# Kernel tuning notes

Hardware: AMD Instinct MI355X
Metric: run time of the kernel (lower is better)

Reference implementation:

```python
import jax, jax.numpy as jnp
import numpy as np

_EPS = 1e-7  # clamp for BCE numerical validity (torch BCE asserts input in [0,1])


def _erode6(m):
    """Binary erosion with 3D 6-connectivity (scipy generate_binary_structure(3,1)),
    border_value=0. m: [B, C, D, H, W] float in {0,1}. Erosion of a binary mask with
    a cross structuring element == min over the voxel and its 6 face neighbors."""
    p = jnp.pad(m, ((0, 0), (0, 0), (1, 1), (1, 1), (1, 1)))  # zero pad == border_value 0
    e = p[:, :, 1:-1, 1:-1, 1:-1]
    e = jnp.minimum(e, p[:, :, :-2, 1:-1, 1:-1])
    e = jnp.minimum(e, p[:, :, 2:, 1:-1, 1:-1])
    e = jnp.minimum(e, p[:, :, 1:-1, :-2, 1:-1])
    e = jnp.minimum(e, p[:, :, 1:-1, 2:, 1:-1])
    e = jnp.minimum(e, p[:, :, 1:-1, 1:-1, :-2])
    e = jnp.minimum(e, p[:, :, 1:-1, 1:-1, 2:])
    return e


def _boundary_map(mask):
    """Faithful to _get_boundary_map: binarize (astype(bool) == nonzero), erode each
    channel, boundary = float_mask - eroded, sum over channels. Returns [B, D, H, W]."""
    mask = mask.astype(jnp.float32)
    mb = (mask != 0).astype(jnp.float32)
    eroded = _erode6(mb)
    return jnp.sum(mask - eroded, axis=1)


def setup_inputs() -> dict:
    key = jax.random.key(0)
    k1, k2 = jax.random.split(key)
    B, C, D, H, W = 4, 2, 128, 192, 192
    inputs = jax.random.normal(k1, (B, C, D, H, W), dtype=jnp.float32)
    targets = jax.random.randint(k2, (B, C, D, H, W), 0, 2, dtype=jnp.int32)
    return {"inputs": inputs, "targets": targets}


def reference(inputs, targets):
    p = jax.nn.sigmoid(inputs)
    boundary_targets = _boundary_map(targets)
    boundary_inputs = _boundary_map(p)
    # binary_cross_entropy(boundary_inputs, boundary_targets, reduction='none')
    bi = jnp.clip(boundary_inputs, _EPS, 1.0 - _EPS)
    loss = -(boundary_targets * jnp.log(bi) + (1.0 - boundary_targets) * jnp.log1p(-bi))
    return jnp.mean(loss)  # reduction='mean'
```

## Files before the change

### kernel.cpp

```cpp
#include <hip/hip_runtime.h>
#include <math.h>

#define Bq 4
#define Dd 128
#define Hh 192
#define Ww 192

typedef unsigned long long ull;

constexpr int HW    = Hh * Ww;
constexpr int DHW   = Dd * HW;
constexpr int CDHW  = 2 * DHW;
constexpr int WPP   = HW / 64;
constexpr int WPC   = Dd * WPP;
constexpr int TOTW  = Bq * 2 * WPC;
constexpr int TOTV  = TOTW * 64;
constexpr float INV_N = 1.0f / 18874368.0f;

#define C0f 1.00000005e-07f
#define C1f 16.1180955f

__device__ __forceinline__ float edge_loss(float x0, float x1, float bt) {
    float p0 = 1.f / (1.f + expf(-x0));
    float p1 = 1.f / (1.f + expf(-x1));
    float bi = fminf(fmaxf(p0 + p1, 1e-7f), 1.f - 1e-7f);
    return -(bt * logf(bi) + (1.f - bt) * log1pf(-bi));
}

__device__ __forceinline__ void block_reduce_atomic(float loss, float* out) {
    #pragma unroll
    for (int off = 32; off > 0; off >>= 1)
        loss += __shfl_down(loss, off, 64);
    __shared__ float s[4];
    int lane = threadIdx.x & 63;
    int wid  = threadIdx.x >> 6;
    if (lane == 0) s[wid] = loss;
    __syncthreads();
    if (threadIdx.x == 0)
        atomicAdd(out, (s[0] + s[1] + s[2] + s[3]) * INV_N);
}

__global__ __launch_bounds__(256) void pack_kernel(
    const int* __restrict__ t, ull* __restrict__ packed)
{
    const int lane  = threadIdx.x & 63;
    const int gwave = (blockIdx.x * 256 + threadIdx.x) >> 6;
    const int base  = gwave * 4096;
    const int* p = t + base + lane;
    ull word = 0;
    #pragma unroll
    for (int k = 0; k < 64; ++k) {
        ull bal = __ballot(p[k * 64] != 0);
        if (lane == k) word = bal;
    }
    packed[gwave * 64 + lane] = word;
}

constexpr int NROWSI = Bq * 126 * 190;

__global__ __launch_bounds__(256) void interior_kernel(
    const float* __restrict__ x, const ull* __restrict__ pk,
    float* __restrict__ out)
{
    int rid = blockIdx.x * 256 + threadIdx.x;
    float loss = 0.f;
    if (rid < NROWSI) {
        int h = 1 + rid % 190;
        int d = 1 + (rid / 190) % 126;
        int b = rid / (190 * 126);

        const ull* q0 = pk + (b * 2) * WPC + d * WPP + h * 3;
        const ull* q1 = q0 + WPC;

        ull c00 = q0[0],   c01 = q0[1],      c02 = q0[2];
        ull n00 = q0[-3],  n01 = q0[-2],     n02 = q0[-1];
        ull s00 = q0[3],   s01 = q0[4],      s02 = q0[5];
        ull f00 = q0[-WPP],f01 = q0[-WPP+1], f02 = q0[-WPP+2];
        ull k00 = q0[WPP], k01 = q0[WPP+1],  k02 = q0[WPP+2];
        ull c10 = q1[0],   c11 = q1[1],      c12 = q1[2];
        ull n10 = q1[-3],  n11 = q1[-2],     n12 = q1[-1];
        ull s10 = q1[3],   s11 = q1[4],      s12 = q1[5];
        ull f10 = q1[-WPP],f11 = q1[-WPP+1], f12 = q1[-WPP+2];
        ull k10 = q1[WPP], k11 = q1[WPP+1],  k12 = q1[WPP+2];

        ull lm00 = c00 << 1, lm01 = (c01 << 1) | (c00 >> 63), lm02 = (c02 << 1) | (c01 >> 63);
        ull rm00 = (c00 >> 1) | (c01 << 63), rm01 = (c01 >> 1) | (c02 << 63), rm02 = c02 >> 1;
        ull lm10 = c10 << 1, lm11 = (c11 << 1) | (c10 >> 63), lm12 = (c12 << 1) | (c11 >> 63);
        ull rm10 = (c10 >> 1) | (c11 << 63), rm11 = (c11 >> 1) | (c12 << 63), rm12 = c12 >> 1;

        ull e00 = c00 & lm00 & rm00 & n00 & s00 & f00 & k00;
        ull e01 = c01 & lm01 & rm01 & n01 & s01 & f01 & k01;
        ull e02 = c02 & lm02 & rm02 & n02 & s02 & f02 & k02;
        ull e10 = c10 & lm10 & rm10 & n10 & s10 & f10 & k10;
        ull e11 = c11 & lm11 & rm11 & n11 & s11 & f11 & k11;
        ull e12 = c12 & lm12 & rm12 & n12 & s12 & f12 & k12;

        int btsum = __popcll(c00) + __popcll(c01) + __popcll(c02)
                  + __popcll(c10) + __popcll(c11) + __popcll(c12)
                  - __popcll(e00) - __popcll(e01) - __popcll(e02)
                  - __popcll(e10) - __popcll(e11) - __popcll(e12);

        int bt_w0   = (int)(c00 & 1)  + (int)(c10 & 1);
        int bt_w191 = (int)(c02 >> 63) + (int)(c12 >> 63);
        int ibt = btsum - bt_w0 - bt_w191;

        int xb = b * CDHW + d * HW + h * Ww;
        loss = fmaf((float)ibt, C1f, 190.f * C0f)
             + edge_loss(x[xb],       x[xb + DHW],       (float)bt_w0)
             + edge_loss(x[xb + 191], x[xb + DHW + 191], (float)bt_w191);
    }
    block_reduce_atomic(loss, out);
}

constexpr int NF1 = Bq * 2 * Hh * 48;
constexpr int NF2 = Bq * 2 * 126 * 48;
constexpr int NF  = NF1 + NF2;

__global__ __launch_bounds__(256) void face_kernel(
    const float* __restrict__ x, const ull* __restrict__ pk,
    float* __restrict__ out)
{
    int fid = blockIdx.x * 256 + threadIdx.x;
    float loss = 0.f;
    if (fid < NF) {
        int b, d, h, q;
        if (fid < NF1) {
            q = fid % 48;
            h = (fid / 48) % Hh;
            d = ((fid / (48 * Hh)) & 1) ? Dd - 1 : 0;
            b = fid / (48 * Hh * 2);
        } else {
            int g = fid - NF1;
            q = g % 48;
            d = 1 + (g / 48) % 126;
            h = ((g / (48 * 126)) & 1) ? Hh - 1 : 0;
            b = g / (48 * 126 * 2);
        }
        int v0  = b * CDHW + d * HW + h * Ww + q * 4;
        int vc0 = (b * 2 * Dd + d) * HW + h * Ww + q * 4;
        float4 xa  = *(const float4*)(x + v0);
        float4 xb4 = *(const float4*)(x + v0 + DHW);
        int sh = vc0 & 63;
        unsigned bits0 = (unsigned)((pk[vc0 >> 6]         >> sh) & 0xFull);
        unsigned bits1 = (unsigned)((pk[(vc0 >> 6) + WPC] >> sh) & 0xFull);
        loss  = edge_loss(xa.x, xb4.x, (float)(( bits0       & 1) + ( bits1       & 1)));
        loss += edge_loss(xa.y, xb4.y, (float)(((bits0 >> 1) & 1) + ((bits1 >> 1) & 1)));
        loss += edge_loss(xa.z, xb4.z, (float)(((bits0 >> 2) & 1) + ((bits1 >> 2) & 1)));
        loss += edge_loss(xa.w, xb4.w, (float)(((bits0 >> 3) & 1) + ((bits1 >> 3) & 1)));
    }
    block_reduce_atomic(loss, out);
}

extern "C" void kernel_launch(void* const* d_in, const int* in_sizes, int n_in,
                              void* d_out, int out_size, void* d_ws, size_t ws_size,
                              hipStream_t stream) {
    const float* x = (const float*)d_in[0];
    const int*   t = (const int*)d_in[1];
    float* out = (float*)d_out;
    ull* packed = (ull*)d_ws;

    hipMemsetAsync(out, 0, sizeof(float), stream);

    pack_kernel<<<TOTV / 16384, 256, 0, stream>>>(t, packed);
    interior_kernel<<<(NROWSI + 255) / 256, 256, 0, stream>>>(x, packed, out);
    face_kernel<<<(NF + 255) / 256, 256, 0, stream>>>(x, packed, out);
}
```

Before: 295.0 us.

## Fuse bit-packing into interior kernel using shared-memory tiles with halo

Removes the separate pack kernel and its global packed buffer; each interior block now ballots a D×H tile plus a one-voxel halo of targets into shared memory and computes the erosion from there. The face kernel reads the int targets directly instead of packed bits. This saves one launch and the global write and re-read of packed words, at the cost of re-reading halo rows (about 9×21 rows per 7×19 tile) and lower occupancy, since only 133 of 256 threads compute.

```diff
diff --git a/kernel.cpp b/kernel.cpp
--- a/kernel.cpp
+++ b/kernel.cpp
@@ -11,11 +11,10 @@
 constexpr int HW    = Hh * Ww;
 constexpr int DHW   = Dd * HW;
 constexpr int CDHW  = 2 * DHW;
-constexpr int WPP   = HW / 64;
-constexpr int WPC   = Dd * WPP;
-constexpr int TOTW  = Bq * 2 * WPC;
-constexpr int TOTV  = TOTW * 64;
 constexpr float INV_N = 1.0f / 18874368.0f;
+
+constexpr int DT = 7,  DSEGN = 18;
+constexpr int HT = 19, HSEGN = 10;
 
 #define C0f 1.00000005e-07f
 #define C1f 16.1180955f
@@ -40,48 +39,58 @@
         atomicAdd(out, (s[0] + s[1] + s[2] + s[3]) * INV_N);
 }
 
-__global__ __launch_bounds__(256) void pack_kernel(
-    const int* __restrict__ t, ull* __restrict__ packed)
+__global__ __launch_bounds__(256) void interior_kernel(
+    const float* __restrict__ x,
+    const int*   __restrict__ t,
+    float*       __restrict__ out)
 {
-    const int lane  = threadIdx.x & 63;
-    const int gwave = (blockIdx.x * 256 + threadIdx.x) >> 6;
-    const int base  = gwave * 4096;
-    const int* p = t + base + lane;
-    ull word = 0;
-    #pragma unroll
-    for (int k = 0; k < 64; ++k) {
-        ull bal = __ballot(p[k * 64] != 0);
-        if (lane == k) word = bal;
+    const int tid  = threadIdx.x;
+    const int hseg = blockIdx.x;
+    const int dseg = blockIdx.y;
+    const int b    = blockIdx.z;
+    const int dlo  = 1 + dseg * DT;
+    const int hlo  = 1 + hseg * HT;
+
+    __shared__ ull pk[DT + 2][HT + 2][2][3];
+
+    const int wave = tid >> 6, lane = tid & 63;
+
+    for (int rs = wave; rs < (DT + 2) * (HT + 2); rs += 4) {
+        int dp = rs / (HT + 2);
+        int hp = rs % (HT + 2);
+        const int* base = t + b * CDHW + (dlo - 1 + dp) * HW
+                            + (hlo - 1 + hp) * Ww + lane;
+        int v0 = base[0],       v1 = base[64],       v2 = base[128];
+        int v3 = base[DHW],     v4 = base[DHW + 64], v5 = base[DHW + 128];
+        ull b0 = __ballot(v0 != 0);
+        ull b1 = __ballot(v1 != 0);
+        ull b2 = __ballot(v2 != 0);
+        ull b3 = __ballot(v3 != 0);
+        ull b4 = __ballot(v4 != 0);
+        ull b5 = __ballot(v5 != 0);
+        if (lane == 0) {
+            pk[dp][hp][0][0] = b0; pk[dp][hp][0][1] = b1; pk[dp][hp][0][2] = b2;
+            pk[dp][hp][1][0] = b3; pk[dp][hp][1][1] = b4; pk[dp][hp][1][2] = b5;
+        }
     }
-    packed[gwave * 64 + lane] = word;
-}
+    __syncthreads();
 
-constexpr int NROWSI = Bq * 126 * 190;
+    float loss = 0.f;
+    if (tid < DT * HT) {
+        int di = tid / HT, hi = tid % HT;
+        int dp = 1 + di,  hp = 1 + hi;
+        int d = dlo + di, h = hlo + hi;
 
-__global__ __launch_bounds__(256) void interior_kernel(
-    const float* __restrict__ x, const ull* __restrict__ pk,
-    float* __restrict__ out)
-{
-    int rid = blockIdx.x * 256 + threadIdx.x;
-    float loss = 0.f;
-    if (rid < NROWSI) {
-        int h = 1 + rid % 190;
-        int d = 1 + (rid / 190) % 126;
-        int b = rid / (190 * 126);
-
-        const ull* q0 = pk + (b * 2) * WPC + d * WPP + h * 3;
-        const ull* q1 = q0 + WPC;
-
-        ull c00 = q0[0],   c01 = q0[1],      c02 = q0[2];
-        ull n00 = q0[-3],  n01 = q0[-2],     n02 = q0[-1];
-        ull s00 = q0[3],   s01 = q0[4],      s02 = q0[5];
-        ull f00 = q0[-WPP],f01 = q0[-WPP+1], f02 = q0[-WPP+2];
-        ull k00 = q0[WPP], k01 = q0[WPP+1],  k02 = q0[WPP+2];
-        ull c10 = q1[0],   c11 = q1[1],      c12 = q1[2];
-        ull n10 = q1[-3],  n11 = q1[-2],     n12 = q1[-1];
-        ull s10 = q1[3],   s11 = q1[4],      s12 = q1[5];
-        ull f10 = q1[-WPP],f11 = q1[-WPP+1], f12 = q1[-WPP+2];
-        ull k10 = q1[WPP], k11 = q1[WPP+1],  k12 = q1[WPP+2];
+        ull c00 = pk[dp][hp][0][0],   c01 = pk[dp][hp][0][1],   c02 = pk[dp][hp][0][2];
+        ull c10 = pk[dp][hp][1][0],   c11 = pk[dp][hp][1][1],   c12 = pk[dp][hp][1][2];
+        ull n00 = pk[dp][hp-1][0][0], n01 = pk[dp][hp-1][0][1], n02 = pk[dp][hp-1][0][2];
+        ull n10 = pk[dp][hp-1][1][0], n11 = pk[dp][hp-1][1][1], n12 = pk[dp][hp-1][1][2];
+        ull s00 = pk[dp][hp+1][0][0], s01 = pk[dp][hp+1][0][1], s02 = pk[dp][hp+1][0][2];
+        ull s10 = pk[dp][hp+1][1][0], s11 = pk[dp][hp+1][1][1], s12 = pk[dp][hp+1][1][2];
+        ull f00 = pk[dp-1][hp][0][0], f01 = pk[dp-1][hp][0][1], f02 = pk[dp-1][hp][0][2];
+        ull f10 = pk[dp-1][hp][1][0], f11 = pk[dp-1][hp][1][1], f12 = pk[dp-1][hp][1][2];
+        ull k00 = pk[dp+1][hp][0][0], k01 = pk[dp+1][hp][0][1], k02 = pk[dp+1][hp][0][2];
+        ull k10 = pk[dp+1][hp][1][0], k11 = pk[dp+1][hp][1][1], k12 = pk[dp+1][hp][1][2];
 
         ull lm00 = c00 << 1, lm01 = (c01 << 1) | (c00 >> 63), lm02 = (c02 << 1) | (c01 >> 63);
         ull rm00 = (c00 >> 1) | (c01 << 63), rm01 = (c01 >> 1) | (c02 << 63), rm02 = c02 >> 1;
@@ -100,7 +109,7 @@
                   - __popcll(e00) - __popcll(e01) - __popcll(e02)
                   - __popcll(e10) - __popcll(e11) - __popcll(e12);
 
-        int bt_w0   = (int)(c00 & 1)  + (int)(c10 & 1);
+        int bt_w0   = (int)(c00 & 1)   + (int)(c10 & 1);
         int bt_w191 = (int)(c02 >> 63) + (int)(c12 >> 63);
         int ibt = btsum - bt_w0 - bt_w191;
 
@@ -117,7 +126,7 @@
 constexpr int NF  = NF1 + NF2;
 
 __global__ __launch_bounds__(256) void face_kernel(
-    const float* __restrict__ x, const ull* __restrict__ pk,
+    const float* __restrict__ x, const int* __restrict__ t,
     float* __restrict__ out)
 {
     int fid = blockIdx.x * 256 + threadIdx.x;
@@ -136,17 +145,15 @@
             h = ((g / (48 * 126)) & 1) ? Hh - 1 : 0;
             b = g / (48 * 126 * 2);
         }
-        int v0  = b * CDHW + d * HW + h * Ww + q * 4;
-        int vc0 = (b * 2 * Dd + d) * HW + h * Ww + q * 4;
+        int v0 = b * CDHW + d * HW + h * Ww + q * 4;
+        int4 t0 = *(const int4*)(t + v0);
+        int4 t1 = *(const int4*)(t + v0 + DHW);
         float4 xa  = *(const float4*)(x + v0);
         float4 xb4 = *(const float4*)(x + v0 + DHW);
-        int sh = vc0 & 63;
-        unsigned bits0 = (unsigned)((pk[vc0 >> 6]         >> sh) & 0xFull);
-        unsigned bits1 = (unsigned)((pk[(vc0 >> 6) + WPC] >> sh) & 0xFull);
-        loss  = edge_loss(xa.x, xb4.x, (float)(( bits0       & 1) + ( bits1       & 1)));
-        loss += edge_loss(xa.y, xb4.y, (float)(((bits0 >> 1) & 1) + ((bits1 >> 1) & 1)));
-        loss += edge_loss(xa.z, xb4.z, (float)(((bits0 >> 2) & 1) + ((bits1 >> 2) & 1)));
-        loss += edge_loss(xa.w, xb4.w, (float)(((bits0 >> 3) & 1) + ((bits1 >> 3) & 1)));
+        loss  = edge_loss(xa.x, xb4.x, (float)(t0.x + t1.x));
+        loss += edge_loss(xa.y, xb4.y, (float)(t0.y + t1.y));
+        loss += edge_loss(xa.z, xb4.z, (float)(t0.z + t1.z));
+        loss += edge_loss(xa.w, xb4.w, (float)(t0.w + t1.w));
     }
     block_reduce_atomic(loss, out);
 }
@@ -157,11 +164,10 @@
     const float* x = (const float*)d_in[0];
     const int*   t = (const int*)d_in[1];
     float* out = (float*)d_out;
-    ull* packed = (ull*)d_ws;
 
     hipMemsetAsync(out, 0, sizeof(float), stream);
 
-    pack_kernel<<<TOTV / 16384, 256, 0, stream>>>(t, packed);
-    interior_kernel<<<(NROWSI + 255) / 256, 256, 0, stream>>>(x, packed, out);
-    face_kernel<<<(NF + 255) / 256, 256, 0, stream>>>(x, packed, out);
+    dim3 grid(HSEGN, DSEGN, Bq);
+    interior_kernel<<<grid, 256, 0, stream>>>(x, t, out);
+    face_kernel<<<(NF + 255) / 256, 256, 0, stream>>>(x, t, out);
 }
```

Result: no change. 294.7 us (-0.1%).
